# Kernel tuning notes

Measured on AMD Instinct MI355X. Metric: run time of the kernel, lower is better.

## Reference

```python
import jax, jax.numpy as jnp
import numpy as np

SHIFT_SIZE = 5
PAD = 2  # shift_size // 2
EPS = 1e-5


def layernorm(x, g, b):
    m = x.mean(-1, keepdims=True)
    v = ((x - m) ** 2).mean(-1, keepdims=True)
    return (x - m) / jnp.sqrt(v + EPS) * g + b


def axial_shift(x, H, W, D, axis):
    # x: (B, N, C) -> torch-style shift along spatial `axis` of (B,C,H,W,D)
    B, N, C = x.shape
    xn = x.transpose(0, 2, 1).reshape(B, C, H, W, D)
    xn = jnp.pad(xn, ((0, 0), (0, 0), (PAD, PAD), (PAD, PAD), (PAD, PAD)))
    cs = -(-C // SHIFT_SIZE)  # torch.chunk uses ceil-sized chunks
    rolled = [
        jnp.roll(xn[:, i * cs:min((i + 1) * cs, C)], s, axis=axis)
        for i, s in enumerate(range(-PAD, PAD + 1))
    ]
    xc = jnp.concatenate(rolled, axis=1)
    xc = xc[:, :, PAD:PAD + H, PAD:PAD + W, PAD:PAD + D]
    return xc.reshape(B, C, H * W * D).transpose(0, 2, 1)


def dwconv3d(x, w, b, H, W, D):
    # x: (B,N,C), w: (C,1,3,3,3) depthwise
    B, N, C = x.shape
    v = x.transpose(0, 2, 1).reshape(B, C, H, W, D)
    y = jax.lax.conv_general_dilated(
        v, w, window_strides=(1, 1, 1), padding=[(1, 1)] * 3,
        dimension_numbers=('NCDHW', 'OIDHW', 'NCDHW'), feature_group_count=C)
    y = y + b[None, :, None, None, None]
    return y.reshape(B, C, N).transpose(0, 2, 1)


def setup_inputs() -> dict:
    key = jax.random.key(0)
    ks = jax.random.split(key, 12)
    C_in, C = 4, 128
    x = jax.random.normal(ks[0], (1, C_in, 96, 96, 96), dtype=jnp.float32)
    p = {
        'x': x,
        'proj_w': jax.random.normal(ks[1], (C, C_in, 3, 3, 3), jnp.float32) * 0.05,
        'proj_b': jnp.zeros((C,), jnp.float32),
        'g0': jnp.ones((C,), jnp.float32), 'b0': jnp.zeros((C,), jnp.float32),
        'g2': jnp.ones((C,), jnp.float32), 'b2': jnp.zeros((C,), jnp.float32),
        'fc1_w': jax.random.normal(ks[2], (C, C), jnp.float32) * 0.02,
        'fc1_b': jnp.zeros((C,), jnp.float32),
        'dw1_w': jax.random.normal(ks[3], (C, 1, 3, 3, 3), jnp.float32) * 0.1,
        'dw1_b': jnp.zeros((C,), jnp.float32),
        'fc2_w': jax.random.normal(ks[4], (C, C), jnp.float32) * 0.02,
        'fc2_b': jnp.zeros((C,), jnp.float32),
        'dw2_w': jax.random.normal(ks[5], (C, 1, 3, 3, 3), jnp.float32) * 0.1,
        'dw2_b': jnp.zeros((C,), jnp.float32),
        'fc3_w': jax.random.normal(ks[6], (C, C), jnp.float32) * 0.02,
        'fc3_b': jnp.zeros((C,), jnp.float32),
        'gn': jnp.ones((C,), jnp.float32), 'bn': jnp.zeros((C,), jnp.float32),
    }
    return p


def reference(x, proj_w, proj_b, g0, b0, g2, b2, fc1_w, fc1_b, dw1_w, dw1_b,
              fc2_w, fc2_b, dw2_w, dw2_b, fc3_w, fc3_b, gn, bn):
    B = x.shape[0]
    # OverlapPatchEmbed: Conv3d(k=3, s=2, p=1)
    v = jax.lax.conv_general_dilated(
        x, proj_w, window_strides=(2, 2, 2), padding=[(1, 1)] * 3,
        dimension_numbers=('NCDHW', 'OIDHW', 'NCDHW'))
    v = v + proj_b[None, :, None, None, None]
    _, C, H, W, D = v.shape
    t = v.reshape(B, C, H * W * D).transpose(0, 2, 1)  # (B,N,C)
    t = layernorm(t, g0, b0)

    # unext_shifted_Block (dropout/droppath in eval -> identity)
    h = layernorm(t, g2, b2)
    h = axial_shift(h, H, W, D, axis=2)
    h = h @ fc1_w.T + fc1_b
    h = dwconv3d(h, dw1_w, dw1_b, H, W, D)
    h = axial_shift(h, H, W, D, axis=3)
    h = h @ fc2_w.T + fc2_b
    h = dwconv3d(h, dw2_w, dw2_b, H, W, D)
    h = axial_shift(h, H, W, D, axis=4)
    h = h @ fc3_w.T + fc3_b
    h = jax.nn.gelu(h, approximate=False)
    t = t + h

    t = layernorm(t, gn, bn)
    out = t.reshape(B, H, W, D, C).transpose(0, 4, 1, 2, 3)
    return out
```

## Files before the change

### kernel.cpp

```cpp
#include <hip/hip_runtime.h>
#include <hip/hip_bf16.h>
#include <math.h>

#define NTOT 110592
#define SD 48
#define SWD 2304

typedef short s16x8 __attribute__((ext_vector_type(8)));
typedef unsigned short u16x8 __attribute__((ext_vector_type(8)));
typedef unsigned short u16x4 __attribute__((ext_vector_type(4)));
typedef float f32x4 __attribute__((ext_vector_type(4)));
typedef unsigned short u16;

__device__ __forceinline__ float bf2f(u16 u) {
    unsigned int x = ((unsigned int)u) << 16;
    float f; __builtin_memcpy(&f, &x, 4); return f;
}
__device__ __forceinline__ u16 f2bf(float f) {
    __hip_bfloat16 h = __float2bfloat16(f);
    u16 u; __builtin_memcpy(&u, &h, 2); return u;
}
__device__ __forceinline__ u16x8 zero8() {
    u16x8 z;
    #pragma unroll
    for (int j = 0; j < 8; ++j) z[j] = 0;
    return z;
}

__device__ __forceinline__ float gelu_f(float x) {
    float y = x * (0.7978845608f + 0.0356774081f * x * x);
    float e = exp2f(y * 2.885390082f);
    return x - x * __builtin_amdgcn_rcpf(e + 1.f);
}

__device__ __forceinline__ u16x8 ld_shift8(const u16* __restrict__ in, int n, int coord,
                                           int STR, int cbase) {
    int g = cbase / 26;
    int split = 26 * (g + 1) - cbase;
    int sh0 = g - 2;
    int cs0 = coord - sh0;
    u16x8 lo = zero8();
    if (cs0 >= 0 && cs0 < SD) lo = *(const u16x8*)&in[(size_t)(n - sh0 * STR) * 128 + cbase];
    if (split >= 8) return lo;
    u16x8 hi = zero8();
    int cs1 = cs0 - 1;
    if (cs1 >= 0 && cs1 < SD) hi = *(const u16x8*)&in[(size_t)(n - (sh0 + 1) * STR) * 128 + cbase];
    u16x8 r;
    #pragma unroll
    for (int j = 0; j < 8; ++j) r[j] = (j < split) ? lo[j] : hi[j];
    return r;
}

__device__ __forceinline__ s16x8 ld_shift8_ln(const u16* __restrict__ t,
                                              const float* __restrict__ mrs,
                                              const float* __restrict__ g2,
                                              const float* __restrict__ b2,
                                              int n, int coord, int STR, int cbase) {
    int g = cbase / 26;
    int split = 26 * (g + 1) - cbase;
    int sh0 = g - 2;
    int cs0 = coord - sh0;
    float gg[8], bb[8];
    {
        f32x4 ga = *(const f32x4*)&g2[cbase];
        f32x4 gb = *(const f32x4*)&g2[cbase + 4];
        f32x4 ba = *(const f32x4*)&b2[cbase];
        f32x4 bbv = *(const f32x4*)&b2[cbase + 4];
        #pragma unroll
        for (int j = 0; j < 4; ++j) {
            gg[j] = ga[j]; gg[j + 4] = gb[j];
            bb[j] = ba[j]; bb[j + 4] = bbv[j];
        }
    }
    float lo[8];
    bool lov = (cs0 >= 0 && cs0 < SD);
    if (lov) {
        int r = n - sh0 * STR;
        u16x8 raw = *(const u16x8*)&t[(size_t)r * 128 + cbase];
        float m = mrs[2 * r], rs = mrs[2 * r + 1];
        #pragma unroll
        for (int j = 0; j < 8; ++j)
            lo[j] = (bf2f(raw[j]) - m) * rs * gg[j] + bb[j];
    } else {
        #pragma unroll
        for (int j = 0; j < 8; ++j) lo[j] = 0.f;
    }
    s16x8 out;
    if (split >= 8) {
        #pragma unroll
        for (int j = 0; j < 8; ++j) out[j] = (short)f2bf(lo[j]);
        return out;
    }
    float hi[8];
    int cs1 = cs0 - 1;
    bool hiv = (cs1 >= 0 && cs1 < SD);
    if (hiv) {
        int r = n - (sh0 + 1) * STR;
        u16x8 raw = *(const u16x8*)&t[(size_t)r * 128 + cbase];
        float m = mrs[2 * r], rs = mrs[2 * r + 1];
        #pragma unroll
        for (int j = 0; j < 8; ++j)
            hi[j] = (bf2f(raw[j]) - m) * rs * gg[j] + bb[j];
    } else {
        #pragma unroll
        for (int j = 0; j < 8; ++j) hi[j] = 0.f;
    }
    #pragma unroll
    for (int j = 0; j < 8; ++j)
        out[j] = (short)f2bf((j < split) ? lo[j] : hi[j]);
    return out;
}

__global__ __launch_bounds__(256) void k_prep(
    const float* __restrict__ pw, const float* __restrict__ fc1w,
    const float* __restrict__ fc2w, const float* __restrict__ fc3w,
    const float* __restrict__ dw1w, const float* __restrict__ dw2w,
    u16* __restrict__ wfP, u16* __restrict__ wf1, u16* __restrict__ wf2,
    u16* __restrict__ wf3, float* __restrict__ dwT1, float* __restrict__ dwT2)
{
    int b = blockIdx.x;
    if (b < 32) {
        int which = b >> 3;
        const float* src = (which == 0) ? pw : (which == 1) ? fc1w : (which == 2) ? fc2w : fc3w;
        u16* dst = (which == 0) ? wfP : (which == 1) ? wf1 : (which == 2) ? wf2 : wf3;
        int idx = (b & 7) * 256 + threadIdx.x;
        int lane = idx & 63;
        int s = (idx >> 6) & 3;
        int t = idx >> 8;
        int co = t * 16 + (lane & 15);
        int kb = s * 32 + (lane >> 4) * 8;
        #pragma unroll
        for (int j = 0; j < 8; ++j) {
            int kk = kb + j;
            float v;
            if (which == 0) {
                int tau = kk >> 2, ci = kk & 3;
                v = (tau < 27) ? src[co * 108 + ci * 27 + tau] : 0.f;
            } else {
                v = src[co * 128 + kk];
            }
            dst[idx * 8 + j] = f2bf(v);
        }
    } else {
        int which = (b - 32) / 14;
        int bb = (b - 32) % 14;
        const float* src = which ? dw2w : dw1w;
        float* dst = which ? dwT2 : dwT1;
        int idx = bb * 256 + threadIdx.x;
        if (idx < 27 * 128) {
            int k = idx >> 7;
            int co = idx & 127;
            dst[idx] = src[co * 27 + k];
        }
    }
}

__global__ __launch_bounds__(256) void k_proj_ln(
    const float* __restrict__ x, const u16* __restrict__ wfrag, const float* __restrict__ pb,
    const float* __restrict__ g0, const float* __restrict__ b0,
    u16* __restrict__ t_out, float* __restrict__ mrs)
{
    __shared__ __align__(16) u16 wfl[16384];
    const int tid = threadIdx.x;
    const int n0 = blockIdx.x * 64;
    const int lane = tid & 63;
    const int wv = tid >> 6;
    const int colb = lane & 15;
    const int q = lane >> 4;

    for (int i = tid; i < 2048; i += 256)
        *(u16x8*)&wfl[i * 8] = *(const u16x8*)&wfrag[i * 8];

    const int arow = wv * 16 + colb;
    const int n = n0 + arow;
    const int oi = n / SWD;
    const int rem = n - oi * SWD;
    const int oj = rem / SD;
    const int ok = rem - oj * SD;
    const int ii0 = 2 * oi - 1, ij0 = 2 * oj - 1, ik0 = 2 * ok - 1;

    s16x8 a4[4];
    #pragma unroll
    for (int s = 0; s < 4; ++s) {
        #pragma unroll
        for (int d = 0; d < 2; ++d) {
            int tq = 2 * q + d;
            int tau = s * 8 + tq;
            u16 v4[4] = {0, 0, 0, 0};
            bool valid = (s < 3) || (tq < 3);
            if (valid) {
                int ti = (tau >= 18 ? 1 : 0) + (tau >= 9 ? 1 : 0);
                int r2 = tau - ti * 9;
                int tj = (r2 >= 6 ? 1 : 0) + (r2 >= 3 ? 1 : 0);
                int tk = r2 - tj * 3;
                int ii = ii0 + ti, ij = ij0 + tj, ik = ik0 + tk;
                if (ii >= 0 && ij >= 0 && ik >= 0) {
                    size_t off = ((size_t)ii * 96 + ij) * 96 + ik;
                    #pragma unroll
                    for (int ci = 0; ci < 4; ++ci)
                        v4[ci] = f2bf(x[(size_t)ci * 884736 + off]);
                }
            }
            a4[s][4 * d + 0] = (short)v4[0]; a4[s][4 * d + 1] = (short)v4[1];
            a4[s][4 * d + 2] = (short)v4[2]; a4[s][4 * d + 3] = (short)v4[3];
        }
    }

    f32x4 acc[8];
    #pragma unroll
    for (int t = 0; t < 8; ++t) {
        float bb = pb[t * 16 + colb];
        acc[t][0] = bb; acc[t][1] = bb; acc[t][2] = bb; acc[t][3] = bb;
    }
    __syncthreads();

    #pragma unroll
    for (int s = 0; s < 4; ++s) {
        s16x8 bf[8];
        #pragma unroll
        for (int t = 0; t < 8; ++t)
            bf[t] = *(const s16x8*)&wfl[((t * 4 + s) * 64 + lane) * 8];
        #pragma unroll
        for (int t = 0; t < 8; ++t)
            acc[t] = __builtin_amdgcn_mfma_f32_16x16x32_bf16(a4[s], bf[t], acc[t], 0, 0, 0);
    }

    float s1[4] = {0.f,0.f,0.f,0.f}, s2[4] = {0.f,0.f,0.f,0.f};
    #pragma unroll
    for (int t = 0; t < 8; ++t)
        #pragma unroll
        for (int r4 = 0; r4 < 4; ++r4) {
            float v = acc[t][r4];
            s1[r4] += v; s2[r4] += v * v;
        }
    #pragma unroll
    for (int r4 = 0; r4 < 4; ++r4)
        #pragma unroll
        for (int m = 1; m < 16; m <<= 1) {
            s1[r4] += __shfl_xor(s1[r4], m);
            s2[r4] += __shfl_xor(s2[r4], m);
        }

    float g0v[8], b0v[8];
    #pragma unroll
    for (int t = 0; t < 8; ++t) {
        int c = t * 16 + colb;
        g0v[t] = g0[c]; b0v[t] = b0[c];
    }

    float tval[8][4];
    float u1[4] = {0.f,0.f,0.f,0.f}, u2[4] = {0.f,0.f,0.f,0.f};
    #pragma unroll
    for (int r4 = 0; r4 < 4; ++r4) {
        float mean = s1[r4] * (1.f / 128.f);
        float var  = fmaxf(s2[r4] * (1.f / 128.f) - mean * mean, 0.f);
        float rstd = rsqrtf(var + 1e-5f);
        #pragma unroll
        for (int t = 0; t < 8; ++t) {
            float tv = (acc[t][r4] - mean) * rstd * g0v[t] + b0v[t];
            tval[t][r4] = tv;
            u1[r4] += tv; u2[r4] += tv * tv;
        }
    }
    #pragma unroll
    for (int r4 = 0; r4 < 4; ++r4) {
        #pragma unroll
        for (int m = 1; m < 16; m <<= 1) {
            u1[r4] += __shfl_xor(u1[r4], m);
            u2[r4] += __shfl_xor(u2[r4], m);
        }
    }

    #pragma unroll
    for (int r4 = 0; r4 < 4; ++r4) {
        float mean2 = u1[r4] * (1.f / 128.f);
        float var2  = fmaxf(u2[r4] * (1.f / 128.f) - mean2 * mean2, 0.f);
        float rstd2 = rsqrtf(var2 + 1e-5f);
        int row = wv * 16 + q * 4 + r4;
        size_t base = (size_t)(n0 + row) * 128;
        #pragma unroll
        for (int t = 0; t < 8; ++t)
            t_out[base + t * 16 + colb] = f2bf(tval[t][r4]);
        if (colb == 0) {
            mrs[2 * (n0 + row) + 0] = mean2;
            mrs[2 * (n0 + row) + 1] = rstd2;
        }
    }
}

__global__ __launch_bounds__(256) void k_shift_mm_ln(
    const u16* __restrict__ tin, const float* __restrict__ mrs,
    const float* __restrict__ g2, const float* __restrict__ b2,
    const u16* __restrict__ wfrag, const float* __restrict__ bias,
    u16* __restrict__ out)
{
    __shared__ __align__(16) u16 wfl[16384];
    const int tid = threadIdx.x;
    const int n0 = blockIdx.x * 64;
    const int lane = tid & 63;
    const int wv = tid >> 6;
    const int colb = lane & 15;
    const int q = lane >> 4;

    for (int i = tid; i < 2048; i += 256)
        *(u16x8*)&wfl[i * 8] = *(const u16x8*)&wfrag[i * 8];

    const int arow = wv * 16 + colb;
    const int n = n0 + arow;
    const int coord = n / SWD;

    s16x8 a4[4];
    #pragma unroll
    for (int s = 0; s < 4; ++s)
        a4[s] = ld_shift8_ln(tin, mrs, g2, b2, n, coord, SWD, s * 32 + q * 8);

    f32x4 acc[8];
    #pragma unroll
    for (int t = 0; t < 8; ++t) {
        float bb = bias[t * 16 + colb];
        acc[t][0] = bb; acc[t][1] = bb; acc[t][2] = bb; acc[t][3] = bb;
    }
    __syncthreads();
    #pragma unroll
    for (int s = 0; s < 4; ++s) {
        s16x8 bf[8];
        #pragma unroll
        for (int t = 0; t < 8; ++t)
            bf[t] = *(const s16x8*)&wfl[((t * 4 + s) * 64 + lane) * 8];
        #pragma unroll
        for (int t = 0; t < 8; ++t)
            acc[t] = __builtin_amdgcn_mfma_f32_16x16x32_bf16(a4[s], bf[t], acc[t], 0, 0, 0);
    }
    #pragma unroll
    for (int r4 = 0; r4 < 4; ++r4) {
        int row = wv * 16 + q * 4 + r4;
        size_t base = (size_t)(n0 + row) * 128;
        #pragma unroll
        for (int t = 0; t < 8; ++t)
            out[base + t * 16 + colb] = f2bf(acc[t][r4]);
    }
}

template <int AXIS>
__global__ __launch_bounds__(256) void k_shift_mm(
    const u16* __restrict__ in, const u16* __restrict__ wfrag, const float* __restrict__ bias,
    u16* __restrict__ out)
{
    __shared__ __align__(16) u16 wfl[16384];
    const int tid = threadIdx.x;
    const int n0 = blockIdx.x * 64;
    const int lane = tid & 63;
    const int wv = tid >> 6;
    const int colb = lane & 15;
    const int q = lane >> 4;

    for (int i = tid; i < 2048; i += 256)
        *(u16x8*)&wfl[i * 8] = *(const u16x8*)&wfrag[i * 8];

    const int arow = wv * 16 + colb;
    const int n = n0 + arow;
    const int STR = (AXIS == 0) ? SWD : (AXIS == 1) ? SD : 1;
    const int coord = (AXIS == 0) ? n / SWD : (AXIS == 1) ? (n / SD) % SD : n % SD;

    s16x8 a4[4];
    #pragma unroll
    for (int s = 0; s < 4; ++s) {
        u16x8 av = ld_shift8(in, n, coord, STR, s * 32 + q * 8);
        a4[s] = *(s16x8*)&av;
    }

    f32x4 acc[8];
    #pragma unroll
    for (int t = 0; t < 8; ++t) {
        float bb = bias[t * 16 + colb];
        acc[t][0] = bb; acc[t][1] = bb; acc[t][2] = bb; acc[t][3] = bb;
    }
    __syncthreads();
    #pragma unroll
    for (int s = 0; s < 4; ++s) {
        s16x8 bf[8];
        #pragma unroll
        for (int t = 0; t < 8; ++t)
            bf[t] = *(const s16x8*)&wfl[((t * 4 + s) * 64 + lane) * 8];
        #pragma unroll
        for (int t = 0; t < 8; ++t)
            acc[t] = __builtin_amdgcn_mfma_f32_16x16x32_bf16(a4[s], bf[t], acc[t], 0, 0, 0);
    }
    #pragma unroll
    for (int r4 = 0; r4 < 4; ++r4) {
        int row = wv * 16 + q * 4 + r4;
        size_t base = (size_t)(n0 + row) * 128;
        #pragma unroll
        for (int t = 0; t < 8; ++t)
            out[base + t * 16 + colb] = f2bf(acc[t][r4]);
    }
}

__global__ __launch_bounds__(256, 4) void k_dw(
    const u16* __restrict__ in, const float* __restrict__ wt, const float* __restrict__ b,
    u16* __restrict__ out)
{
    __shared__ __align__(16) float wtl[27 * 128];
    const int tid = threadIdx.x;
    const int cg = tid & 15;
    const int kq = tid >> 4;
    const int k0 = kq * 3;
    const int bid = blockIdx.x;
    const int ij = (bid & 7) * 288 + (bid >> 3);
    const int i = ij / SD;
    const int j = ij - i * SD;
    const int c = cg * 8;

    for (int t = tid; t < 864; t += 256)
        ((float4*)wtl)[t] = ((const float4*)wt)[t];

    const int kclamp0 = (k0 - 1 < 0) ? 0 : (k0 - 1);
    const int kclamp4 = (k0 + 3 > SD - 1) ? (SD - 1) : (k0 + 3);
    const bool k0bad = (k0 - 1 < 0);
    const bool k4bad = (k0 + 3 > SD - 1);

    float acc[3][8];
    {
        float4 ba = *(const float4*)&b[c];
        float4 bb = *(const float4*)&b[c + 4];
        #pragma unroll
        for (int t = 0; t < 3; ++t) {
            acc[t][0] = ba.x; acc[t][1] = ba.y; acc[t][2] = ba.z; acc[t][3] = ba.w;
            acc[t][4] = bb.x; acc[t][5] = bb.y; acc[t][6] = bb.z; acc[t][7] = bb.w;
        }
    }

    bool okt[9];
    const u16* baseptr[9];
    #pragma unroll
    for (int t9 = 0; t9 < 9; ++t9) {
        int di = t9 / 3 - 1, dj = t9 % 3 - 1;
        int ii = i + di, jj = j + dj;
        okt[t9] = ((unsigned)ii < SD) && ((unsigned)jj < SD);
        int iic = (ii < 0) ? 0 : (ii > SD - 1 ? SD - 1 : ii);
        int jjc = (jj < 0) ? 0 : (jj > SD - 1 ? SD - 1 : jj);
        baseptr[t9] = &in[(size_t)((iic * SD + jjc) * SD) * 128 + c];
    }

    u16x8 win[2][5];
    {
        const u16* base = baseptr[0];
        win[0][0] = *(const u16x8*)(base + (size_t)kclamp0 * 128);
        win[0][1] = *(const u16x8*)(base + (size_t)(k0    ) * 128);
        win[0][2] = *(const u16x8*)(base + (size_t)(k0 + 1) * 128);
        win[0][3] = *(const u16x8*)(base + (size_t)(k0 + 2) * 128);
        win[0][4] = *(const u16x8*)(base + (size_t)kclamp4 * 128);
    }
    __syncthreads();

    #pragma unroll
    for (int t9 = 0; t9 < 9; ++t9) {
        const int cur = t9 & 1;
        if (t9 < 8) {
            const u16* base = baseptr[t9 + 1];
            win[cur ^ 1][0] = *(const u16x8*)(base + (size_t)kclamp0 * 128);
            win[cur ^ 1][1] = *(const u16x8*)(base + (size_t)(k0    ) * 128);
            win[cur ^ 1][2] = *(const u16x8*)(base + (size_t)(k0 + 1) * 128);
            win[cur ^ 1][3] = *(const u16x8*)(base + (size_t)(k0 + 2) * 128);
            win[cur ^ 1][4] = *(const u16x8*)(base + (size_t)kclamp4 * 128);
        }
        if (okt[t9]) {
            const int tap0 = t9 * 3;
            float wv[3][8];
            #pragma unroll
            for (int dk = 0; dk < 3; ++dk) {
                float4 wa = *(const float4*)&wtl[(tap0 + dk) * 128 + c];
                float4 wb = *(const float4*)&wtl[(tap0 + dk) * 128 + c + 4];
                wv[dk][0] = wa.x; wv[dk][1] = wa.y; wv[dk][2] = wa.z; wv[dk][3] = wa.w;
                wv[dk][4] = wb.x; wv[dk][5] = wb.y; wv[dk][6] = wb.z; wv[dk][7] = wb.w;
            }
            #pragma unroll
            for (int s = 0; s < 5; ++s) {
                bool bad = (s == 0 && k0bad) || (s == 4 && k4bad);
                float vs[8];
                #pragma unroll
                for (int m = 0; m < 8; ++m)
                    vs[m] = bad ? 0.f : bf2f(win[cur][s][m]);
                #pragma unroll
                for (int t = 0; t < 3; ++t) {
                    int dk = s - t;
                    if (dk >= 0 && dk < 3) {
                        #pragma unroll
                        for (int m = 0; m < 8; ++m)
                            acc[t][m] = fmaf(wv[dk][m], vs[m], acc[t][m]);
                    }
                }
            }
        }
    }
    #pragma unroll
    for (int t = 0; t < 3; ++t) {
        u16x8 o;
        #pragma unroll
        for (int m = 0; m < 8; ++m) o[m] = f2bf(acc[t][m]);
        *(u16x8*)&out[(size_t)((i * SD + j) * SD + k0 + t) * 128 + c] = o;
    }
}

__global__ __launch_bounds__(256) void k_final(
    const u16* __restrict__ in, const u16* __restrict__ wfrag, const float* __restrict__ bias,
    const u16* __restrict__ tin, const float* __restrict__ gn, const float* __restrict__ bn,
    float* __restrict__ out)
{
    __shared__ __align__(16) unsigned char smem[34816];
    u16* wfl = (u16*)smem;
    float* Osm = (float*)smem;
    const int tid = threadIdx.x;
    const int n0 = blockIdx.x * 64;
    const int lane = tid & 63;
    const int wv = tid >> 6;
    const int colb = lane & 15;
    const int q = lane >> 4;

    for (int i = tid; i < 2048; i += 256)
        *(u16x8*)&wfl[i * 8] = *(const u16x8*)&wfrag[i * 8];

    const int nn = wv * 16 + colb;
    const int n = n0 + nn;
    const int coord = n % SD;

    u16x4 tq[8];
    #pragma unroll
    for (int ta = 0; ta < 8; ++ta)
        tq[ta] = *(const u16x4*)&tin[(size_t)n * 128 + ta * 16 + q * 4];
    s16x8 b4[4];
    #pragma unroll
    for (int s = 0; s < 4; ++s) {
        u16x8 bv = ld_shift8(in, n, coord, 1, s * 32 + q * 8);
        b4[s] = *(s16x8*)&bv;
    }

    f32x4 acc[8];
    #pragma unroll
    for (int ta = 0; ta < 8; ++ta)
        #pragma unroll
        for (int r4 = 0; r4 < 4; ++r4)
            acc[ta][r4] = bias[ta * 16 + q * 4 + r4];
    __syncthreads();

    #pragma unroll
    for (int s = 0; s < 4; ++s) {
        s16x8 af[8];
        #pragma unroll
        for (int ta = 0; ta < 8; ++ta)
            af[ta] = *(const s16x8*)&wfl[((ta * 4 + s) * 64 + lane) * 8];
        #pragma unroll
        for (int ta = 0; ta < 8; ++ta)
            acc[ta] = __builtin_amdgcn_mfma_f32_16x16x32_bf16(af[ta], b4[s], acc[ta], 0, 0, 0);
    }

    float s1 = 0.f, s2 = 0.f;
    #pragma unroll
    for (int ta = 0; ta < 8; ++ta)
        #pragma unroll
        for (int r4 = 0; r4 < 4; ++r4) {
            float v = gelu_f(acc[ta][r4]) + bf2f(tq[ta][r4]);
            acc[ta][r4] = v;
            s1 += v; s2 += v * v;
        }
    s1 += __shfl_xor(s1, 16); s2 += __shfl_xor(s2, 16);
    s1 += __shfl_xor(s1, 32); s2 += __shfl_xor(s2, 32);
    float mean = s1 * (1.f / 128.f);
    float var  = fmaxf(s2 * (1.f / 128.f) - mean * mean, 0.f);
    float rstd = rsqrtf(var + 1e-5f);

    __syncthreads();

    #pragma unroll
    for (int ta = 0; ta < 8; ++ta)
        #pragma unroll
        for (int r4 = 0; r4 < 4; ++r4) {
            int co = ta * 16 + q * 4 + r4;
            float o = (acc[ta][r4] - mean) * rstd * gn[co] + bn[co];
            Osm[co * 68 + nn] = o;
        }
    __syncthreads();

    #pragma unroll
    for (int it = 0; it < 8; ++it) {
        int idx = it * 256 + tid;
        int row = idx >> 4;
        int c4 = idx & 15;
        f32x4 v = *(const f32x4*)&Osm[row * 68 + c4 * 4];
        *(f32x4*)&out[(size_t)row * NTOT + n0 + c4 * 4] = v;
    }
}

extern "C" void kernel_launch(void* const* d_in, const int* in_sizes, int n_in,
                              void* d_out, int out_size, void* d_ws, size_t ws_size,
                              hipStream_t stream)
{
    const float* x    = (const float*)d_in[0];
    const float* pw   = (const float*)d_in[1];
    const float* pb   = (const float*)d_in[2];
    const float* g0   = (const float*)d_in[3];
    const float* b0   = (const float*)d_in[4];
    const float* g2   = (const float*)d_in[5];
    const float* b2   = (const float*)d_in[6];
    const float* fc1w = (const float*)d_in[7];
    const float* fc1b = (const float*)d_in[8];
    const float* dw1w = (const float*)d_in[9];
    const float* dw1b = (const float*)d_in[10];
    const float* fc2w = (const float*)d_in[11];
    const float* fc2b = (const float*)d_in[12];
    const float* dw2w = (const float*)d_in[13];
    const float* dw2b = (const float*)d_in[14];
    const float* fc3w = (const float*)d_in[15];
    const float* fc3b = (const float*)d_in[16];
    const float* gn   = (const float*)d_in[17];
    const float* bn   = (const float*)d_in[18];
    float* out = (float*)d_out;

    u16* tbuf = (u16*)d_ws;
    u16* h1   = tbuf + (size_t)NTOT * 128;
    u16* h2   = h1 + (size_t)NTOT * 128;
    u16* wfP  = h2 + (size_t)NTOT * 128;
    u16* wf1  = wfP + 16384;
    u16* wf2  = wf1 + 16384;
    u16* wf3  = wf2 + 16384;
    float* dwT1 = (float*)(wf3 + 16384);
    float* dwT2 = dwT1 + 27 * 128;
    float* mrs  = dwT2 + 27 * 128;

    k_prep<<<60, 256, 0, stream>>>(pw, fc1w, fc2w, fc3w, dw1w, dw2w,
                                   wfP, wf1, wf2, wf3, dwT1, dwT2);

    k_proj_ln<<<NTOT / 64, 256, 0, stream>>>(x, wfP, pb, g0, b0, tbuf, mrs);
    k_shift_mm_ln<<<NTOT / 64, 256, 0, stream>>>(tbuf, mrs, g2, b2, wf1, fc1b, h2);
    k_dw<<<SWD, 256, 0, stream>>>(h2, dwT1, dw1b, h1);
    k_shift_mm<1><<<NTOT / 64, 256, 0, stream>>>(h1, wf2, fc2b, h2);
    k_dw<<<SWD, 256, 0, stream>>>(h2, dwT2, dw2b, h1);
    k_final<<<NTOT / 64, 256, 0, stream>>>(h1, wf3, fc3b, tbuf, gn, bn, out);
}
```

Measured before the change: 148.8 us.

## Process four row tiles per block with software-prefetched gathers in proj and final kernels

k_proj_ln and k_final now loop over four 64-row sub-tiles per block, loading the weight fragments into shared memory once and prefetching the next sub-tile's inputs into registers while the current one runs MFMAs. The grid shrinks fourfold. This aims to amortize the weight staging and hide gather latency. k_final also drops its LDS transpose and writes output directly with 64-byte segments per row, which may reduce store coalescing and raises register pressure.

After: 201.3 us. 35.3% more time.

```diff
diff --git a/kernel.cpp b/kernel.cpp
--- a/kernel.cpp
+++ b/kernel.cpp
@@ -109,6 +109,40 @@
     for (int j = 0; j < 8; ++j)
         out[j] = (short)f2bf((j < split) ? lo[j] : hi[j]);
     return out;
+}
+
+__device__ __forceinline__ void proj_gather(const float* __restrict__ x, int n, int q,
+                                            s16x8 a4[4]) {
+    int oi = n / SWD;
+    int rem = n - oi * SWD;
+    int oj = rem / SD;
+    int ok = rem - oj * SD;
+    int ii0 = 2 * oi - 1, ij0 = 2 * oj - 1, ik0 = 2 * ok - 1;
+    #pragma unroll
+    for (int s = 0; s < 4; ++s) {
+        #pragma unroll
+        for (int d = 0; d < 2; ++d) {
+            int tq = 2 * q + d;
+            int tau = s * 8 + tq;
+            u16 v4[4] = {0, 0, 0, 0};
+            bool valid = (s < 3) || (tq < 3);
+            if (valid) {
+                int ti = (tau >= 18 ? 1 : 0) + (tau >= 9 ? 1 : 0);
+                int r2 = tau - ti * 9;
+                int tj = (r2 >= 6 ? 1 : 0) + (r2 >= 3 ? 1 : 0);
+                int tk = r2 - tj * 3;
+                int ii = ii0 + ti, ij = ij0 + tj, ik = ik0 + tk;
+                if (ii >= 0 && ij >= 0 && ik >= 0) {
+                    size_t off = ((size_t)ii * 96 + ij) * 96 + ik;
+                    #pragma unroll
+                    for (int ci = 0; ci < 4; ++ci)
+                        v4[ci] = f2bf(x[(size_t)ci * 884736 + off]);
+                }
+            }
+            a4[s][4 * d + 0] = (short)v4[0]; a4[s][4 * d + 1] = (short)v4[1];
+            a4[s][4 * d + 2] = (short)v4[2]; a4[s][4 * d + 3] = (short)v4[3];
+        }
+    }
 }
 
 __global__ __launch_bounds__(256) void k_prep(
@@ -162,129 +196,104 @@
 {
     __shared__ __align__(16) u16 wfl[16384];
     const int tid = threadIdx.x;
-    const int n0 = blockIdx.x * 64;
+    const int nb = blockIdx.x * 256;
     const int lane = tid & 63;
     const int wv = tid >> 6;
     const int colb = lane & 15;
     const int q = lane >> 4;
+    const int arow = wv * 16 + colb;
 
     for (int i = tid; i < 2048; i += 256)
         *(u16x8*)&wfl[i * 8] = *(const u16x8*)&wfrag[i * 8];
 
-    const int arow = wv * 16 + colb;
-    const int n = n0 + arow;
-    const int oi = n / SWD;
-    const int rem = n - oi * SWD;
-    const int oj = rem / SD;
-    const int ok = rem - oj * SD;
-    const int ii0 = 2 * oi - 1, ij0 = 2 * oj - 1, ik0 = 2 * ok - 1;
-
-    s16x8 a4[4];
-    #pragma unroll
-    for (int s = 0; s < 4; ++s) {
-        #pragma unroll
-        for (int d = 0; d < 2; ++d) {
-            int tq = 2 * q + d;
-            int tau = s * 8 + tq;
-            u16 v4[4] = {0, 0, 0, 0};
-            bool valid = (s < 3) || (tq < 3);
-            if (valid) {
-                int ti = (tau >= 18 ? 1 : 0) + (tau >= 9 ? 1 : 0);
-                int r2 = tau - ti * 9;
-                int tj = (r2 >= 6 ? 1 : 0) + (r2 >= 3 ? 1 : 0);
-                int tk = r2 - tj * 3;
-                int ii = ii0 + ti, ij = ij0 + tj, ik = ik0 + tk;
-                if (ii >= 0 && ij >= 0 && ik >= 0) {
-                    size_t off = ((size_t)ii * 96 + ij) * 96 + ik;
-                    #pragma unroll
-                    for (int ci = 0; ci < 4; ++ci)
-                        v4[ci] = f2bf(x[(size_t)ci * 884736 + off]);
-                }
-            }
-            a4[s][4 * d + 0] = (short)v4[0]; a4[s][4 * d + 1] = (short)v4[1];
-            a4[s][4 * d + 2] = (short)v4[2]; a4[s][4 * d + 3] = (short)v4[3];
-        }
-    }
-
-    f32x4 acc[8];
-    #pragma unroll
-    for (int t = 0; t < 8; ++t) {
-        float bb = pb[t * 16 + colb];
-        acc[t][0] = bb; acc[t][1] = bb; acc[t][2] = bb; acc[t][3] = bb;
-    }
-    __syncthreads();
-
-    #pragma unroll
-    for (int s = 0; s < 4; ++s) {
-        s16x8 bf[8];
-        #pragma unroll
-        for (int t = 0; t < 8; ++t)
-            bf[t] = *(const s16x8*)&wfl[((t * 4 + s) * 64 + lane) * 8];
-        #pragma unroll
-        for (int t = 0; t < 8; ++t)
-            acc[t] = __builtin_amdgcn_mfma_f32_16x16x32_bf16(a4[s], bf[t], acc[t], 0, 0, 0);
-    }
-
-    float s1[4] = {0.f,0.f,0.f,0.f}, s2[4] = {0.f,0.f,0.f,0.f};
-    #pragma unroll
-    for (int t = 0; t < 8; ++t)
-        #pragma unroll
-        for (int r4 = 0; r4 < 4; ++r4) {
-            float v = acc[t][r4];
-            s1[r4] += v; s2[r4] += v * v;
-        }
-    #pragma unroll
-    for (int r4 = 0; r4 < 4; ++r4)
-        #pragma unroll
-        for (int m = 1; m < 16; m <<= 1) {
-            s1[r4] += __shfl_xor(s1[r4], m);
-            s2[r4] += __shfl_xor(s2[r4], m);
-        }
-
-    float g0v[8], b0v[8];
+    float pbr[8], g0v[8], b0v[8];
     #pragma unroll
     for (int t = 0; t < 8; ++t) {
         int c = t * 16 + colb;
-        g0v[t] = g0[c]; b0v[t] = b0[c];
-    }
-
-    float tval[8][4];
-    float u1[4] = {0.f,0.f,0.f,0.f}, u2[4] = {0.f,0.f,0.f,0.f};
-    #pragma unroll
-    for (int r4 = 0; r4 < 4; ++r4) {
-        float mean = s1[r4] * (1.f / 128.f);
-        float var  = fmaxf(s2[r4] * (1.f / 128.f) - mean * mean, 0.f);
-        float rstd = rsqrtf(var + 1e-5f);
+        pbr[t] = pb[c]; g0v[t] = g0[c]; b0v[t] = b0[c];
+    }
+
+    s16x8 a4[4], a4n[4];
+    proj_gather(x, nb + arow, q, a4);
+    __syncthreads();
+
+    #pragma unroll
+    for (int sub = 0; sub < 4; ++sub) {
+        const int n0 = nb + sub * 64;
+        if (sub < 3) proj_gather(x, n0 + 64 + arow, q, a4n);
+
+        f32x4 acc[8];
         #pragma unroll
         for (int t = 0; t < 8; ++t) {
-            float tv = (acc[t][r4] - mean) * rstd * g0v[t] + b0v[t];
-            tval[t][r4] = tv;
-            u1[r4] += tv; u2[r4] += tv * tv;
-        }
-    }
-    #pragma unroll
-    for (int r4 = 0; r4 < 4; ++r4) {
-        #pragma unroll
-        for (int m = 1; m < 16; m <<= 1) {
-            u1[r4] += __shfl_xor(u1[r4], m);
-            u2[r4] += __shfl_xor(u2[r4], m);
-        }
-    }
-
-    #pragma unroll
-    for (int r4 = 0; r4 < 4; ++r4) {
-        float mean2 = u1[r4] * (1.f / 128.f);
-        float var2  = fmaxf(u2[r4] * (1.f / 128.f) - mean2 * mean2, 0.f);
-        float rstd2 = rsqrtf(var2 + 1e-5f);
-        int row = wv * 16 + q * 4 + r4;
-        size_t base = (size_t)(n0 + row) * 128;
+            acc[t][0] = pbr[t]; acc[t][1] = pbr[t]; acc[t][2] = pbr[t]; acc[t][3] = pbr[t];
+        }
+        #pragma unroll
+        for (int s = 0; s < 4; ++s) {
+            s16x8 bf[8];
+            #pragma unroll
+            for (int t = 0; t < 8; ++t)
+                bf[t] = *(const s16x8*)&wfl[((t * 4 + s) * 64 + lane) * 8];
+            #pragma unroll
+            for (int t = 0; t < 8; ++t)
+                acc[t] = __builtin_amdgcn_mfma_f32_16x16x32_bf16(a4[s], bf[t], acc[t], 0, 0, 0);
+        }
+
+        float s1[4] = {0.f,0.f,0.f,0.f}, s2[4] = {0.f,0.f,0.f,0.f};
         #pragma unroll
         for (int t = 0; t < 8; ++t)
-            t_out[base + t * 16 + colb] = f2bf(tval[t][r4]);
-        if (colb == 0) {
-            mrs[2 * (n0 + row) + 0] = mean2;
-            mrs[2 * (n0 + row) + 1] = rstd2;
-        }
+            #pragma unroll
+            for (int r4 = 0; r4 < 4; ++r4) {
+                float v = acc[t][r4];
+                s1[r4] += v; s2[r4] += v * v;
+            }
+        #pragma unroll
+        for (int r4 = 0; r4 < 4; ++r4)
+            #pragma unroll
+            for (int m = 1; m < 16; m <<= 1) {
+                s1[r4] += __shfl_xor(s1[r4], m);
+                s2[r4] += __shfl_xor(s2[r4], m);
+            }
+
+        float tval[8][4];
+        float u1[4] = {0.f,0.f,0.f,0.f}, u2[4] = {0.f,0.f,0.f,0.f};
+        #pragma unroll
+        for (int r4 = 0; r4 < 4; ++r4) {
+            float mean = s1[r4] * (1.f / 128.f);
+            float var  = fmaxf(s2[r4] * (1.f / 128.f) - mean * mean, 0.f);
+            float rstd = rsqrtf(var + 1e-5f);
+            #pragma unroll
+            for (int t = 0; t < 8; ++t) {
+                float tv = (acc[t][r4] - mean) * rstd * g0v[t] + b0v[t];
+                tval[t][r4] = tv;
+                u1[r4] += tv; u2[r4] += tv * tv;
+            }
+        }
+        #pragma unroll
+        for (int r4 = 0; r4 < 4; ++r4) {
+            #pragma unroll
+            for (int m = 1; m < 16; m <<= 1) {
+                u1[r4] += __shfl_xor(u1[r4], m);
+                u2[r4] += __shfl_xor(u2[r4], m);
+            }
+        }
+
+        #pragma unroll
+        for (int r4 = 0; r4 < 4; ++r4) {
+            float mean2 = u1[r4] * (1.f / 128.f);
+            float var2  = fmaxf(u2[r4] * (1.f / 128.f) - mean2 * mean2, 0.f);
+            float rstd2 = rsqrtf(var2 + 1e-5f);
+            int row = wv * 16 + q * 4 + r4;
+            size_t base = (size_t)(n0 + row) * 128;
+            #pragma unroll
+            for (int t = 0; t < 8; ++t)
+                t_out[base + t * 16 + colb] = f2bf(tval[t][r4]);
+            if (colb == 0) {
+                mrs[2 * (n0 + row) + 0] = mean2;
+                mrs[2 * (n0 + row) + 1] = rstd2;
+            }
+        }
+        #pragma unroll
+        for (int s = 0; s < 4; ++s) a4[s] = a4n[s];
     }
 }
 
@@ -507,87 +516,107 @@
     const u16* __restrict__ tin, const float* __restrict__ gn, const float* __restrict__ bn,
     float* __restrict__ out)
 {
-    __shared__ __align__(16) unsigned char smem[34816];
-    u16* wfl = (u16*)smem;
-    float* Osm = (float*)smem;
+    __shared__ __align__(16) u16 wfl[16384];
     const int tid = threadIdx.x;
-    const int n0 = blockIdx.x * 64;
+    const int nb = blockIdx.x * 256;
     const int lane = tid & 63;
     const int wv = tid >> 6;
     const int colb = lane & 15;
     const int q = lane >> 4;
+    const int nn = wv * 16 + colb;
 
     for (int i = tid; i < 2048; i += 256)
         *(u16x8*)&wfl[i * 8] = *(const u16x8*)&wfrag[i * 8];
 
-    const int nn = wv * 16 + colb;
-    const int n = n0 + nn;
-    const int coord = n % SD;
-
-    u16x4 tq[8];
+    f32x4 bias4[8];
     #pragma unroll
     for (int ta = 0; ta < 8; ++ta)
-        tq[ta] = *(const u16x4*)&tin[(size_t)n * 128 + ta * 16 + q * 4];
-    s16x8 b4[4];
-    #pragma unroll
-    for (int s = 0; s < 4; ++s) {
-        u16x8 bv = ld_shift8(in, n, coord, 1, s * 32 + q * 8);
-        b4[s] = *(s16x8*)&bv;
-    }
-
-    f32x4 acc[8];
-    #pragma unroll
-    for (int ta = 0; ta < 8; ++ta)
         #pragma unroll
         for (int r4 = 0; r4 < 4; ++r4)
-            acc[ta][r4] = bias[ta * 16 + q * 4 + r4];
-    __syncthreads();
-
-    #pragma unroll
-    for (int s = 0; s < 4; ++s) {
-        s16x8 af[8];
-        #pragma unroll
-        for (int ta = 0; ta < 8; ++ta)
-            af[ta] = *(const s16x8*)&wfl[((ta * 4 + s) * 64 + lane) * 8];
-        #pragma unroll
-        for (int ta = 0; ta < 8; ++ta)
-            acc[ta] = __builtin_amdgcn_mfma_f32_16x16x32_bf16(af[ta], b4[s], acc[ta], 0, 0, 0);
-    }
-
-    float s1 = 0.f, s2 = 0.f;
-    #pragma unroll
-    for (int ta = 0; ta < 8; ++ta)
-        #pragma unroll
-        for (int r4 = 0; r4 < 4; ++r4) {
-            float v = gelu_f(acc[ta][r4]) + bf2f(tq[ta][r4]);
-            acc[ta][r4] = v;
-            s1 += v; s2 += v * v;
-        }
-    s1 += __shfl_xor(s1, 16); s2 += __shfl_xor(s2, 16);
-    s1 += __shfl_xor(s1, 32); s2 += __shfl_xor(s2, 32);
-    float mean = s1 * (1.f / 128.f);
-    float var  = fmaxf(s2 * (1.f / 128.f) - mean * mean, 0.f);
-    float rstd = rsqrtf(var + 1e-5f);
-
-    __syncthreads();
-
+            bias4[ta][r4] = bias[ta * 16 + q * 4 + r4];
+    float gnv[8][4], bnv[8][4];
     #pragma unroll
     for (int ta = 0; ta < 8; ++ta)
         #pragma unroll
         for (int r4 = 0; r4 < 4; ++r4) {
             int co = ta * 16 + q * 4 + r4;
-            float o = (acc[ta][r4] - mean) * rstd * gn[co] + bn[co];
-            Osm[co * 68 + nn] = o;
-        }
+            gnv[ta][r4] = gn[co]; bnv[ta][r4] = bn[co];
+        }
+
+    u16x4 tq[8], tqn[8];
+    s16x8 b4[4], b4n[4];
+    {
+        int n = nb + nn;
+        int coord = n % SD;
+        #pragma unroll
+        for (int ta = 0; ta < 8; ++ta)
+            tq[ta] = *(const u16x4*)&tin[(size_t)n * 128 + ta * 16 + q * 4];
+        #pragma unroll
+        for (int s = 0; s < 4; ++s) {
+            u16x8 bv = ld_shift8(in, n, coord, 1, s * 32 + q * 8);
+            b4[s] = *(s16x8*)&bv;
+        }
+    }
     __syncthreads();
 
     #pragma unroll
-    for (int it = 0; it < 8; ++it) {
-        int idx = it * 256 + tid;
-        int row = idx >> 4;
-        int c4 = idx & 15;
-        f32x4 v = *(const f32x4*)&Osm[row * 68 + c4 * 4];
-        *(f32x4*)&out[(size_t)row * NTOT + n0 + c4 * 4] = v;
+    for (int sub = 0; sub < 4; ++sub) {
+        const int n = nb + sub * 64 + nn;
+        if (sub < 3) {
+            int n2 = n + 64;
+            int coord2 = n2 % SD;
+            #pragma unroll
+            for (int ta = 0; ta < 8; ++ta)
+                tqn[ta] = *(const u16x4*)&tin[(size_t)n2 * 128 + ta * 16 + q * 4];
+            #pragma unroll
+            for (int s = 0; s < 4; ++s) {
+                u16x8 bv = ld_shift8(in, n2, coord2, 1, s * 32 + q * 8);
+                b4n[s] = *(s16x8*)&bv;
+            }
+        }
+
+        f32x4 acc[8];
+        #pragma unroll
+        for (int ta = 0; ta < 8; ++ta) acc[ta] = bias4[ta];
+        #pragma unroll
+        for (int s = 0; s < 4; ++s) {
+            s16x8 af[8];
+            #pragma unroll
+            for (int ta = 0; ta < 8; ++ta)
+                af[ta] = *(const s16x8*)&wfl[((ta * 4 + s) * 64 + lane) * 8];
+            #pragma unroll
+            for (int ta = 0; ta < 8; ++ta)
+                acc[ta] = __builtin_amdgcn_mfma_f32_16x16x32_bf16(af[ta], b4[s], acc[ta], 0, 0, 0);
+        }
+
+        float s1 = 0.f, s2 = 0.f;
+        #pragma unroll
+        for (int ta = 0; ta < 8; ++ta)
+            #pragma unroll
+            for (int r4 = 0; r4 < 4; ++r4) {
+                float v = gelu_f(acc[ta][r4]) + bf2f(tq[ta][r4]);
+                acc[ta][r4] = v;
+                s1 += v; s2 += v * v;
+            }
+        s1 += __shfl_xor(s1, 16); s2 += __shfl_xor(s2, 16);
+        s1 += __shfl_xor(s1, 32); s2 += __shfl_xor(s2, 32);
+        float mean = s1 * (1.f / 128.f);
+        float var  = fmaxf(s2 * (1.f / 128.f) - mean * mean, 0.f);
+        float rstd = rsqrtf(var + 1e-5f);
+
+        #pragma unroll
+        for (int ta = 0; ta < 8; ++ta)
+            #pragma unroll
+            for (int r4 = 0; r4 < 4; ++r4) {
+                int co = ta * 16 + q * 4 + r4;
+                float o = (acc[ta][r4] - mean) * rstd * gnv[ta][r4] + bnv[ta][r4];
+                out[(size_t)co * NTOT + n] = o;
+            }
+
+        #pragma unroll
+        for (int ta = 0; ta < 8; ++ta) tq[ta] = tqn[ta];
+        #pragma unroll
+        for (int s = 0; s < 4; ++s) b4[s] = b4n[s];
     }
 }
 
@@ -630,10 +659,10 @@
     k_prep<<<60, 256, 0, stream>>>(pw, fc1w, fc2w, fc3w, dw1w, dw2w,
                                    wfP, wf1, wf2, wf3, dwT1, dwT2);
 
-    k_proj_ln<<<NTOT / 64, 256, 0, stream>>>(x, wfP, pb, g0, b0, tbuf, mrs);
+    k_proj_ln<<<NTOT / 256, 256, 0, stream>>>(x, wfP, pb, g0, b0, tbuf, mrs);
     k_shift_mm_ln<<<NTOT / 64, 256, 0, stream>>>(tbuf, mrs, g2, b2, wf1, fc1b, h2);
     k_dw<<<SWD, 256, 0, stream>>>(h2, dwT1, dw1b, h1);
     k_shift_mm<1><<<NTOT / 64, 256, 0, stream>>>(h1, wf2, fc2b, h2);
     k_dw<<<SWD, 256, 0, stream>>>(h2, dwT2, dw2b, h1);
-    k_final<<<NTOT / 64, 256, 0, stream>>>(h1, wf3, fc3b, tbuf, gn, bn, out);
-}
+    k_final<<<NTOT / 256, 256, 0, stream>>>(h1, wf3, fc3b, tbuf, gn, bn, out);
+}
```
